# Optimization experiments

Hardware: AMD Instinct MI355X
Metric: run time of the kernel (lower is better)

Reference implementation:

```python
import jax, jax.numpy as jnp
import numpy as np

D_MODEL = 1024
N_HEADS = 16
D_K = D_MODEL // N_HEADS


def setup_inputs() -> dict:
    key = jax.random.key(0)
    ks = jax.random.split(key, 9)
    B, S, D = 2, 2048, D_MODEL
    q = jax.random.normal(ks[0], (B, S, D), dtype=jnp.float32)
    v = jax.random.normal(ks[1], (B, S, D), dtype=jnp.float32)
    k = jax.random.normal(ks[2], (B, S, D), dtype=jnp.float32)
    att_mask = jnp.zeros((B, S, S), dtype=jnp.float32)
    seq_mask = jax.random.uniform(ks[3], (B, S, S), dtype=jnp.float32)
    scale = 1.0 / np.sqrt(D)
    Wq = jax.random.normal(ks[4], (D, D), dtype=jnp.float32) * scale
    Wk = jax.random.normal(ks[5], (D, D), dtype=jnp.float32) * scale
    Wv = jax.random.normal(ks[6], (D, D), dtype=jnp.float32) * scale
    Wo = jax.random.normal(ks[7], (D, D), dtype=jnp.float32) * scale
    return {"q": q, "v": v, "k": k, "att_mask": att_mask, "seq_mask": seq_mask,
            "Wq": Wq, "Wk": Wk, "Wv": Wv, "Wo": Wo}


def _split_heads(x, B):
    # [B, S, D] -> [B, H, S, d_k]
    return x.reshape(B, -1, N_HEADS, D_K).transpose(0, 2, 1, 3)


def reference(q, v, k, att_mask, seq_mask, Wq, Wk, Wv, Wo):
    B = q.shape[0]
    qh = _split_heads(q @ Wq, B)
    kh = _split_heads(k @ Wk, B)
    vh = _split_heads(v @ Wv, B)
    # scores: [B, H, Sq, Sk]
    scores = jnp.einsum('bhqd,bhkd->bhqk', qh, kh) / jnp.sqrt(jnp.float32(D_K))
    scores = scores + att_mask[:, None]
    attn = jax.nn.softmax(scores, axis=-1)
    attn = attn * seq_mask[:, None]  # post-softmax multiplicative mask
    out = jnp.einsum('bhqk,bhkd->bhqd', attn, vh)
    out = out.transpose(0, 2, 1, 3).reshape(B, -1, D_MODEL)
    return out @ Wo
```

## Files before the change

kernel.cpp:

```cpp
#include <hip/hip_runtime.h>
#include <cstddef>

typedef __attribute__((ext_vector_type(8))) short s16x8;
typedef __attribute__((ext_vector_type(4))) float f32x4;
typedef __attribute__((ext_vector_type(4))) unsigned short us4;

static __device__ __forceinline__ float bf2f(unsigned short u) {
    union { unsigned u; float f; } v;
    v.u = ((unsigned)u) << 16;
    return v.f;
}

static __device__ __forceinline__ unsigned short f2bf(float f) {
    union { float f; unsigned u; } v;
    v.f = f;
    unsigned r = v.u + 0x7fffu + ((v.u >> 16) & 1u);
    return (unsigned short)(r >> 16);
}

static __device__ __forceinline__ float ldf(const unsigned short* p, size_t i) { return bf2f(p[i]); }
static __device__ __forceinline__ float ldf(const float* p, size_t i) { return p[i]; }
static __device__ __forceinline__ void stf(unsigned short* p, size_t i, float v) { p[i] = f2bf(v); }
static __device__ __forceinline__ void stf(float* p, size_t i, float v) { p[i] = v; }

__global__ __launch_bounds__(256) void probe_dtype(
    const unsigned short* __restrict__ q, unsigned* __restrict__ flags)
{
    __shared__ float red[256];
    const int t = threadIdx.x;
    float m = 0.0f;
    for (int i = t; i < 16384; i += 256) {
        float x = fabsf(bf2f(q[i]));
        if (!(x == x)) x = 1.0e30f;
        m = fmaxf(m, x);
    }
    red[t] = m;
    __syncthreads();
    for (int s = 128; s > 0; s >>= 1) {
        if (t < s) red[t] = fmaxf(red[t], red[t + s]);
        __syncthreads();
    }
    if (t == 0) {
        flags[0] = (red[0] < 1000.0f) ? 0u : 1u;
        flags[1] = 0u;
    }
}

__global__ __launch_bounds__(256) void probe_zero(
    const uint4* __restrict__ m, unsigned* __restrict__ flags)
{
    const unsigned dt = flags[0];
    const size_t n = dt ? 2097152u : 1048576u;
    unsigned acc = 0;
    for (size_t i = (size_t)blockIdx.x * 256 + threadIdx.x; i < n;
         i += (size_t)gridDim.x * 256) {
        uint4 v = m[i];
        acc |= v.x | v.y | v.z | v.w;
    }
    if (acc) atomicOr(&flags[1], 1u);
}

__global__ __launch_bounds__(256) void cvt_f32_bf16(
    const float4* __restrict__ src, us4* __restrict__ dst, unsigned n4,
    const unsigned* __restrict__ flags, unsigned gate)
{
    if (flags[0] != 1u) return;
    if (gate != 0u && flags[1] == 0u) return;
    for (unsigned i = blockIdx.x * 256u + threadIdx.x; i < n4;
         i += gridDim.x * 256u) {
        float4 v = src[i];
        us4 o;
        o.x = f2bf(v.x); o.y = f2bf(v.y); o.z = f2bf(v.z); o.w = f2bf(v.w);
        dst[i] = o;
    }
}

__global__ __launch_bounds__(256) void copy_bf16(
    const uint4* __restrict__ src, uint4* __restrict__ dst, unsigned n16,
    const unsigned* __restrict__ flags, unsigned gate)
{
    if (flags[0] != 0u) return;
    if (gate != 0u && flags[1] == 0u) return;
    for (unsigned i = blockIdx.x * 256u + threadIdx.x; i < n16;
         i += gridDim.x * 256u)
        dst[i] = src[i];
}

template <typename T>
__global__ __launch_bounds__(256) void transpose_w(
    const T* __restrict__ src, unsigned short* __restrict__ dst,
    const unsigned* __restrict__ flag, unsigned want)
{
    if (*flag != want) return;
    __shared__ unsigned short tile[32][33];
    const int c0 = blockIdx.x * 32, r0 = blockIdx.y * 32;
    const int tx = threadIdx.x, ty = threadIdx.y;
#pragma unroll
    for (int i = 0; i < 32; i += 8)
        tile[ty + i][tx] = f2bf(ldf(src, (size_t)(r0 + ty + i) * 1024 + c0 + tx));
    __syncthreads();
#pragma unroll
    for (int i = 0; i < 32; i += 8)
        dst[(size_t)(c0 + ty + i) * 1024 + r0 + tx] = tile[tx][ty + i];
}

template <typename TO>
__global__ __launch_bounds__(256) void gemm_kernel(
    const unsigned short* __restrict__ A, const unsigned short* __restrict__ Bt,
    TO* __restrict__ out, int mode, const unsigned* __restrict__ flags, unsigned want)
{
    if (want != 2u && flags[0] != want) return;
    const int K = 1024;
    __shared__ __align__(16) unsigned short lA[64 * 72];
    __shared__ __align__(16) unsigned short lB[64 * 72];

    const int m0 = blockIdx.y * 64, n0 = blockIdx.x * 64;
    const int t = threadIdx.x;
    const int w = t >> 6, l = t & 63, quad = l >> 4, l15 = l & 15;
    const int srow = t >> 2, scol = (t & 3) * 16;

    f32x4 acc[4] = {};

    for (int k0 = 0; k0 < K; k0 += 64) {
        const uint4* ga = (const uint4*)(A + (size_t)(m0 + srow) * K + k0 + scol);
        uint4 a0 = ga[0], a1 = ga[1];
        const uint4* gb = (const uint4*)(Bt + (size_t)(n0 + srow) * K + k0 + scol);
        uint4 b0 = gb[0], b1 = gb[1];
        *(uint4*)&lA[srow * 72 + scol] = a0;
        *(uint4*)&lA[srow * 72 + scol + 8] = a1;
        *(uint4*)&lB[srow * 72 + scol] = b0;
        *(uint4*)&lB[srow * 72 + scol + 8] = b1;
        __syncthreads();
#pragma unroll
        for (int kk = 0; kk < 64; kk += 32) {
            s16x8 af = *(const s16x8*)&lA[(w * 16 + l15) * 72 + kk + quad * 8];
#pragma unroll
            for (int g = 0; g < 4; g++) {
                s16x8 bf = *(const s16x8*)&lB[(g * 16 + l15) * 72 + kk + quad * 8];
                acc[g] = __builtin_amdgcn_mfma_f32_16x16x32_bf16(af, bf, acc[g], 0, 0, 0);
            }
        }
        __syncthreads();
    }

#pragma unroll
    for (int g = 0; g < 4; g++) {
#pragma unroll
        for (int r = 0; r < 4; r++) {
            int row = m0 + w * 16 + quad * 4 + r;
            int col = n0 + g * 16 + l15;
            float val = acc[g][r];
            if (mode == 0) {
                stf(out, (size_t)row * 1024 + col, val);
            } else {
                int b = row >> 11, s = row & 2047;
                int h = col >> 6, d = col & 63;
                if (mode == 1)
                    stf(out, (((size_t)(b * 16 + h) * 2048) + s) * 64 + d, val);
                else
                    stf(out, (((size_t)(b * 16 + h) * 64) + d) * 2048 + s, val);
            }
        }
    }
}

template <typename TM>
__global__ __launch_bounds__(256) void attn_kernel(
    const unsigned short* __restrict__ qh, const unsigned short* __restrict__ kh,
    const unsigned short* __restrict__ vt, const TM* __restrict__ amask,
    const unsigned short* __restrict__ smask, unsigned short* __restrict__ aout,
    const unsigned* __restrict__ flags, unsigned want)
{
    if (flags[0] != want) return;
    const bool useA = (flags[1] != 0u);
    const int S = 2048, DK = 64, H = 16;
    const int qt = blockIdx.x, h = blockIdx.y, b = blockIdx.z;
    const unsigned short* qhb = qh + (size_t)(b * H + h) * S * DK;
    const unsigned short* khb = kh + (size_t)(b * H + h) * S * DK;
    const unsigned short* vtb = vt + (size_t)(b * H + h) * DK * S;
    const TM* amb = amask + (size_t)b * S * S;
    const unsigned short* smb = smask + (size_t)b * S * S;

    __shared__ __align__(16) unsigned short lK[64 * 72];
    __shared__ __align__(16) unsigned short lV[64 * 72];
    __shared__ __align__(16) unsigned short lP[4][16 * 72];

    const int t = threadIdx.x;
    const int w = t >> 6, l = t & 63, quad = l >> 4, l15 = l & 15;
    const int q0 = qt * 64;
    const int srow = t >> 2, scol = (t & 3) * 16;

    const int qrow_a = q0 + w * 16 + l15;
    s16x8 qf0 = *(const s16x8*)&qhb[(size_t)qrow_a * DK + quad * 8];
    s16x8 qf1 = *(const s16x8*)&qhb[(size_t)qrow_a * DK + 32 + quad * 8];

    float mrun[4], lrun[4];
    f32x4 o[4] = {};
#pragma unroll
    for (int r = 0; r < 4; r++) { mrun[r] = -INFINITY; lrun[r] = 0.0f; }

    for (int k0 = 0; k0 < S; k0 += 64) {
        const uint4* gk = (const uint4*)&khb[(size_t)(k0 + srow) * DK + scol];
        const uint4* gv = (const uint4*)&vtb[(size_t)srow * S + k0 + scol];
        uint4 ka = gk[0], kb = gk[1];
        uint4 va = gv[0], vb = gv[1];
        *(uint4*)&lK[srow * 72 + scol] = ka;
        *(uint4*)&lK[srow * 72 + scol + 8] = kb;
        *(uint4*)&lV[srow * 72 + scol] = va;
        *(uint4*)&lV[srow * 72 + scol + 8] = vb;
        __syncthreads();

        f32x4 sc[4] = {};
#pragma unroll
        for (int kk = 0; kk < 64; kk += 32) {
            s16x8 af = (kk == 0) ? qf0 : qf1;
#pragma unroll
            for (int g = 0; g < 4; g++) {
                s16x8 bf = *(const s16x8*)&lK[(g * 16 + l15) * 72 + kk + quad * 8];
                sc[g] = __builtin_amdgcn_mfma_f32_16x16x32_bf16(af, bf, sc[g], 0, 0, 0);
            }
        }

#pragma unroll
        for (int r = 0; r < 4; r++) {
            const int qr = q0 + w * 16 + quad * 4 + r;
            const size_t mrow = (size_t)qr * S + k0;
            float sv[4];
            float mx = -INFINITY;
            if (useA) {
#pragma unroll
                for (int g = 0; g < 4; g++) {
                    float s = sc[g][r] * 0.125f + ldf(amb, mrow + g * 16 + l15);
                    sv[g] = s;
                    mx = fmaxf(mx, s);
                }
            } else {
#pragma unroll
                for (int g = 0; g < 4; g++) {
                    float s = sc[g][r] * 0.125f;
                    sv[g] = s;
                    mx = fmaxf(mx, s);
                }
            }
#pragma unroll
            for (int d = 1; d < 16; d <<= 1) mx = fmaxf(mx, __shfl_xor(mx, d));
            float mnew = fmaxf(mrun[r], mx);
            float rs = 0.0f;
#pragma unroll
            for (int g = 0; g < 4; g++) {
                float e = __expf(sv[g] - mnew);
                sv[g] = e;
                rs += e;
            }
#pragma unroll
            for (int d = 1; d < 16; d <<= 1) rs += __shfl_xor(rs, d);
            float alpha = __expf(mrun[r] - mnew);
            lrun[r] = lrun[r] * alpha + rs;
            mrun[r] = mnew;
#pragma unroll
            for (int g = 0; g < 4; g++) o[g][r] *= alpha;
#pragma unroll
            for (int g = 0; g < 4; g++) {
                float pm = sv[g] * bf2f(smb[mrow + g * 16 + l15]);
                lP[w][(quad * 4 + r) * 72 + g * 16 + l15] = f2bf(pm);
            }
        }
        __syncthreads();

#pragma unroll
        for (int kk = 0; kk < 64; kk += 32) {
            s16x8 pf = *(const s16x8*)&lP[w][l15 * 72 + kk + quad * 8];
#pragma unroll
            for (int g = 0; g < 4; g++) {
                s16x8 vf = *(const s16x8*)&lV[(g * 16 + l15) * 72 + kk + quad * 8];
                o[g] = __builtin_amdgcn_mfma_f32_16x16x32_bf16(pf, vf, o[g], 0, 0, 0);
            }
        }
        __syncthreads();
    }

#pragma unroll
    for (int r = 0; r < 4; r++) {
        float inv = 1.0f / lrun[r];
        const int qr = q0 + w * 16 + quad * 4 + r;
#pragma unroll
        for (int g = 0; g < 4; g++) {
            aout[((size_t)(b * S + qr)) * 1024 + h * 64 + g * 16 + l15] =
                f2bf(o[g][r] * inv);
        }
    }
}

extern "C" void kernel_launch(void* const* d_in, const int* in_sizes, int n_in,
                              void* d_out, int out_size, void* d_ws, size_t ws_size,
                              hipStream_t stream)
{
    const void* q   = d_in[0];
    const void* v   = d_in[1];
    const void* k   = d_in[2];
    const void* att = d_in[3];
    const void* seq = d_in[4];
    const void* Wq  = d_in[5];
    const void* Wk  = d_in[6];
    const void* Wv  = d_in[7];
    const void* Wo  = d_in[8];

    const size_t WELEM = 1024 * 1024;
    const size_t HELEM = (size_t)2 * 16 * 2048 * 64;

    unsigned* flags = (unsigned*)d_ws;
    unsigned short* base = (unsigned short*)((char*)d_ws + 512);
    unsigned short* r0 = base;
    unsigned short* qh = base + HELEM;
    unsigned short* kh = qh + HELEM;
    unsigned short* vt = kh + HELEM;
    unsigned short* qb = vt + HELEM;
    unsigned short* kb = qb + HELEM;
    unsigned short* vb = kb + HELEM;
    unsigned short* seqb = qb;

    const dim3 tg(32, 32), tb(32, 8);
    const dim3 gg(16, 64), gb(256);
    const dim3 ag(32, 16, 2), ab(256);

    probe_dtype<<<1, 256, 0, stream>>>((const unsigned short*)q, flags);
    probe_zero<<<1024, 256, 0, stream>>>((const uint4*)att, flags);

    const unsigned n4h = 1048576u, n16h = 524288u;
    cvt_f32_bf16<<<1024, 256, 0, stream>>>((const float4*)q, (us4*)qb, n4h, flags, 0);
    cvt_f32_bf16<<<1024, 256, 0, stream>>>((const float4*)k, (us4*)kb, n4h, flags, 0);
    cvt_f32_bf16<<<1024, 256, 0, stream>>>((const float4*)v, (us4*)vb, n4h, flags, 0);
    copy_bf16<<<1024, 256, 0, stream>>>((const uint4*)q, (uint4*)qb, n16h, flags, 0);
    copy_bf16<<<1024, 256, 0, stream>>>((const uint4*)k, (uint4*)kb, n16h, flags, 0);
    copy_bf16<<<1024, 256, 0, stream>>>((const uint4*)v, (uint4*)vb, n16h, flags, 0);

    transpose_w<unsigned short><<<tg, tb, 0, stream>>>((const unsigned short*)Wq, r0 + 0 * WELEM, flags, 0);
    transpose_w<unsigned short><<<tg, tb, 0, stream>>>((const unsigned short*)Wk, r0 + 1 * WELEM, flags, 0);
    transpose_w<unsigned short><<<tg, tb, 0, stream>>>((const unsigned short*)Wv, r0 + 2 * WELEM, flags, 0);
    transpose_w<float><<<tg, tb, 0, stream>>>((const float*)Wq, r0 + 0 * WELEM, flags, 1);
    transpose_w<float><<<tg, tb, 0, stream>>>((const float*)Wk, r0 + 1 * WELEM, flags, 1);
    transpose_w<float><<<tg, tb, 0, stream>>>((const float*)Wv, r0 + 2 * WELEM, flags, 1);

    gemm_kernel<unsigned short><<<gg, gb, 0, stream>>>(qb, r0 + 0 * WELEM, qh, 1, flags, 2);
    gemm_kernel<unsigned short><<<gg, gb, 0, stream>>>(kb, r0 + 1 * WELEM, kh, 1, flags, 2);
    gemm_kernel<unsigned short><<<gg, gb, 0, stream>>>(vb, r0 + 2 * WELEM, vt, 2, flags, 2);

    const unsigned n4s = 2097152u, n16s = 1048576u;
    cvt_f32_bf16<<<2048, 256, 0, stream>>>((const float4*)seq, (us4*)seqb, n4s, flags, 0);
    copy_bf16<<<2048, 256, 0, stream>>>((const uint4*)seq, (uint4*)seqb, n16s, flags, 0);

    unsigned short* ao = r0;
    attn_kernel<unsigned short><<<ag, ab, 0, stream>>>(qh, kh, vt, (const unsigned short*)att, seqb, ao, flags, 0);
    attn_kernel<float><<<ag, ab, 0, stream>>>(qh, kh, vt, (const float*)att, seqb, ao, flags, 1);

    transpose_w<unsigned short><<<tg, tb, 0, stream>>>((const unsigned short*)Wo, qh, flags, 0);
    transpose_w<float><<<tg, tb, 0, stream>>>((const float*)Wo, qh, flags, 1);

    gemm_kernel<unsigned short><<<gg, gb, 0, stream>>>(ao, qh, (unsigned short*)d_out, 0, flags, 0);
    gemm_kernel<float><<<gg, gb, 0, stream>>>(ao, qh, (float*)d_out, 0, flags, 1);
}
```

Before: 435.9 us.

## Fuse launches, use exp2 softmax with lazy rescale and swizzled P tile

Merges the three conversion, copy and weight-transpose launches into single multi-operand kernels. The bf16 path now reads the seq mask directly and skips its copy. In attention, the scale is folded into a log2 domain so exp2 can be used. The running max is rescaled only when some lane's max grows, and row sums are reduced once at the end. The P tile in LDS uses an XOR swizzle, and bf16 packing uses the hardware convert instruction. These cut launch overhead, ALU/shuffle work and LDS bank conflicts, at the cost of a different rounding path.

```diff
diff --git a/kernel.cpp b/kernel.cpp
--- a/kernel.cpp
+++ b/kernel.cpp
@@ -17,6 +17,18 @@
     unsigned r = v.u + 0x7fffu + ((v.u >> 16) & 1u);
     return (unsigned short)(r >> 16);
 }
+
+static __device__ __forceinline__ unsigned short f2bf_fast(float f) {
+    unsigned r;
+    asm("v_cvt_pk_bf16_f32 %0, %1, %2" : "=v"(r) : "v"(f), "v"(f));
+    return (unsigned short)r;
+}
+
+#if __has_builtin(__builtin_amdgcn_exp2f)
+#define EXP2F(x) __builtin_amdgcn_exp2f(x)
+#else
+#define EXP2F(x) exp2f(x)
+#endif
 
 static __device__ __forceinline__ float ldf(const unsigned short* p, size_t i) { return bf2f(p[i]); }
 static __device__ __forceinline__ float ldf(const float* p, size_t i) { return p[i]; }
@@ -60,12 +72,43 @@
     if (acc) atomicOr(&flags[1], 1u);
 }
 
+__global__ __launch_bounds__(256) void cvt3_f32_bf16(
+    const float4* __restrict__ s0, us4* __restrict__ d0,
+    const float4* __restrict__ s1, us4* __restrict__ d1,
+    const float4* __restrict__ s2, us4* __restrict__ d2,
+    unsigned n4, const unsigned* __restrict__ flags)
+{
+    if (flags[0] != 1u) return;
+    const float4* s = (blockIdx.y == 0) ? s0 : (blockIdx.y == 1) ? s1 : s2;
+    us4* d = (blockIdx.y == 0) ? d0 : (blockIdx.y == 1) ? d1 : d2;
+    for (unsigned i = blockIdx.x * 256u + threadIdx.x; i < n4;
+         i += gridDim.x * 256u) {
+        float4 v = s[i];
+        us4 o;
+        o.x = f2bf(v.x); o.y = f2bf(v.y); o.z = f2bf(v.z); o.w = f2bf(v.w);
+        d[i] = o;
+    }
+}
+
+__global__ __launch_bounds__(256) void copy3_bf16(
+    const uint4* __restrict__ s0, uint4* __restrict__ d0,
+    const uint4* __restrict__ s1, uint4* __restrict__ d1,
+    const uint4* __restrict__ s2, uint4* __restrict__ d2,
+    unsigned n16, const unsigned* __restrict__ flags)
+{
+    if (flags[0] != 0u) return;
+    const uint4* s = (blockIdx.y == 0) ? s0 : (blockIdx.y == 1) ? s1 : s2;
+    uint4* d = (blockIdx.y == 0) ? d0 : (blockIdx.y == 1) ? d1 : d2;
+    for (unsigned i = blockIdx.x * 256u + threadIdx.x; i < n16;
+         i += gridDim.x * 256u)
+        d[i] = s[i];
+}
+
 __global__ __launch_bounds__(256) void cvt_f32_bf16(
     const float4* __restrict__ src, us4* __restrict__ dst, unsigned n4,
-    const unsigned* __restrict__ flags, unsigned gate)
+    const unsigned* __restrict__ flags)
 {
     if (flags[0] != 1u) return;
-    if (gate != 0u && flags[1] == 0u) return;
     for (unsigned i = blockIdx.x * 256u + threadIdx.x; i < n4;
          i += gridDim.x * 256u) {
         float4 v = src[i];
@@ -75,23 +118,34 @@
     }
 }
 
-__global__ __launch_bounds__(256) void copy_bf16(
-    const uint4* __restrict__ src, uint4* __restrict__ dst, unsigned n16,
-    const unsigned* __restrict__ flags, unsigned gate)
-{
-    if (flags[0] != 0u) return;
-    if (gate != 0u && flags[1] == 0u) return;
-    for (unsigned i = blockIdx.x * 256u + threadIdx.x; i < n16;
-         i += gridDim.x * 256u)
-        dst[i] = src[i];
-}
-
 template <typename T>
 __global__ __launch_bounds__(256) void transpose_w(
     const T* __restrict__ src, unsigned short* __restrict__ dst,
     const unsigned* __restrict__ flag, unsigned want)
 {
     if (*flag != want) return;
+    __shared__ unsigned short tile[32][33];
+    const int c0 = blockIdx.x * 32, r0 = blockIdx.y * 32;
+    const int tx = threadIdx.x, ty = threadIdx.y;
+#pragma unroll
+    for (int i = 0; i < 32; i += 8)
+        tile[ty + i][tx] = f2bf(ldf(src, (size_t)(r0 + ty + i) * 1024 + c0 + tx));
+    __syncthreads();
+#pragma unroll
+    for (int i = 0; i < 32; i += 8)
+        dst[(size_t)(c0 + ty + i) * 1024 + r0 + tx] = tile[tx][ty + i];
+}
+
+template <typename T>
+__global__ __launch_bounds__(256) void transpose_w3(
+    const T* __restrict__ s0, const T* __restrict__ s1, const T* __restrict__ s2,
+    unsigned short* __restrict__ d0, unsigned short* __restrict__ d1,
+    unsigned short* __restrict__ d2,
+    const unsigned* __restrict__ flag, unsigned want)
+{
+    if (*flag != want) return;
+    const T* src = (blockIdx.z == 0) ? s0 : (blockIdx.z == 1) ? s1 : s2;
+    unsigned short* dst = (blockIdx.z == 0) ? d0 : (blockIdx.z == 1) ? d1 : d2;
     __shared__ unsigned short tile[32][33];
     const int c0 = blockIdx.x * 32, r0 = blockIdx.y * 32;
     const int tx = threadIdx.x, ty = threadIdx.y;
@@ -178,8 +232,6 @@
     const unsigned short* qhb = qh + (size_t)(b * H + h) * S * DK;
     const unsigned short* khb = kh + (size_t)(b * H + h) * S * DK;
     const unsigned short* vtb = vt + (size_t)(b * H + h) * DK * S;
-    const TM* amb = amask + (size_t)b * S * S;
-    const unsigned short* smb = smask + (size_t)b * S * S;
 
     __shared__ __align__(16) unsigned short lK[64 * 72];
     __shared__ __align__(16) unsigned short lV[64 * 72];
@@ -190,14 +242,26 @@
     const int q0 = qt * 64;
     const int srow = t >> 2, scol = (t & 3) * 16;
 
+    const float SCALE2 = 0.18033688011112042f;
+    const float LOG2E  = 1.4426950408889634f;
+
+    const unsigned short* mr[4];
+    const TM* ar[4];
+#pragma unroll
+    for (int r = 0; r < 4; r++) {
+        const size_t rowoff = (size_t)(q0 + w * 16 + quad * 4 + r) * S + l15;
+        mr[r] = smask + (size_t)b * S * S + rowoff;
+        ar[r] = amask + (size_t)b * S * S + rowoff;
+    }
+
     const int qrow_a = q0 + w * 16 + l15;
     s16x8 qf0 = *(const s16x8*)&qhb[(size_t)qrow_a * DK + quad * 8];
     s16x8 qf1 = *(const s16x8*)&qhb[(size_t)qrow_a * DK + 32 + quad * 8];
 
-    float mrun[4], lrun[4];
+    float mrun[4], lsum[4];
     f32x4 o[4] = {};
 #pragma unroll
-    for (int r = 0; r < 4; r++) { mrun[r] = -INFINITY; lrun[r] = 0.0f; }
+    for (int r = 0; r < 4; r++) { mrun[r] = -INFINITY; lsum[r] = 0.0f; }
 
     for (int k0 = 0; k0 < S; k0 += 64) {
         const uint4* gk = (const uint4*)&khb[(size_t)(k0 + srow) * DK + scol];
@@ -223,53 +287,47 @@
 
 #pragma unroll
         for (int r = 0; r < 4; r++) {
-            const int qr = q0 + w * 16 + quad * 4 + r;
-            const size_t mrow = (size_t)qr * S + k0;
             float sv[4];
-            float mx = -INFINITY;
             if (useA) {
 #pragma unroll
-                for (int g = 0; g < 4; g++) {
-                    float s = sc[g][r] * 0.125f + ldf(amb, mrow + g * 16 + l15);
-                    sv[g] = s;
-                    mx = fmaxf(mx, s);
-                }
+                for (int g = 0; g < 4; g++)
+                    sv[g] = fmaf((float)ldf(ar[r], k0 + g * 16), LOG2E,
+                                 sc[g][r] * SCALE2);
             } else {
 #pragma unroll
-                for (int g = 0; g < 4; g++) {
-                    float s = sc[g][r] * 0.125f;
-                    sv[g] = s;
-                    mx = fmaxf(mx, s);
-                }
-            }
+                for (int g = 0; g < 4; g++) sv[g] = sc[g][r] * SCALE2;
+            }
+            float mx = fmaxf(fmaxf(sv[0], sv[1]), fmaxf(sv[2], sv[3]));
 #pragma unroll
             for (int d = 1; d < 16; d <<= 1) mx = fmaxf(mx, __shfl_xor(mx, d));
-            float mnew = fmaxf(mrun[r], mx);
-            float rs = 0.0f;
-#pragma unroll
-            for (int g = 0; g < 4; g++) {
-                float e = __expf(sv[g] - mnew);
-                sv[g] = e;
-                rs += e;
-            }
-#pragma unroll
-            for (int d = 1; d < 16; d <<= 1) rs += __shfl_xor(rs, d);
-            float alpha = __expf(mrun[r] - mnew);
-            lrun[r] = lrun[r] * alpha + rs;
-            mrun[r] = mnew;
-#pragma unroll
-            for (int g = 0; g < 4; g++) o[g][r] *= alpha;
-#pragma unroll
-            for (int g = 0; g < 4; g++) {
-                float pm = sv[g] * bf2f(smb[mrow + g * 16 + l15]);
-                lP[w][(quad * 4 + r) * 72 + g * 16 + l15] = f2bf(pm);
-            }
-        }
-        __syncthreads();
-
+
+            if (!__all(mx <= mrun[r])) {
+                float mnew = fmaxf(mrun[r], mx);
+                float alpha = EXP2F(mrun[r] - mnew);
+                lsum[r] *= alpha;
+#pragma unroll
+                for (int g = 0; g < 4; g++) o[g][r] *= alpha;
+                mrun[r] = mnew;
+            }
+
+            const int rowp = quad * 4 + r;
+            const int rsw = (rowp & 8) << 1;
+            float e0 = EXP2F(sv[0] - mrun[r]);
+            float e1 = EXP2F(sv[1] - mrun[r]);
+            float e2 = EXP2F(sv[2] - mrun[r]);
+            float e3 = EXP2F(sv[3] - mrun[r]);
+            lsum[r] += (e0 + e1) + (e2 + e3);
+            lP[w][rowp * 72 + ((0 * 16 + l15) ^ rsw)] = f2bf_fast(e0 * bf2f(mr[r][k0 + 0]));
+            lP[w][rowp * 72 + ((1 * 16 + l15) ^ rsw)] = f2bf_fast(e1 * bf2f(mr[r][k0 + 16]));
+            lP[w][rowp * 72 + ((2 * 16 + l15) ^ rsw)] = f2bf_fast(e2 * bf2f(mr[r][k0 + 32]));
+            lP[w][rowp * 72 + ((3 * 16 + l15) ^ rsw)] = f2bf_fast(e3 * bf2f(mr[r][k0 + 48]));
+        }
+        __syncthreads();
+
+        const int rdsw = (l15 & 8) << 1;
 #pragma unroll
         for (int kk = 0; kk < 64; kk += 32) {
-            s16x8 pf = *(const s16x8*)&lP[w][l15 * 72 + kk + quad * 8];
+            s16x8 pf = *(const s16x8*)&lP[w][l15 * 72 + ((kk + quad * 8) ^ rdsw)];
 #pragma unroll
             for (int g = 0; g < 4; g++) {
                 s16x8 vf = *(const s16x8*)&lV[(g * 16 + l15) * 72 + kk + quad * 8];
@@ -281,12 +339,15 @@
 
 #pragma unroll
     for (int r = 0; r < 4; r++) {
-        float inv = 1.0f / lrun[r];
+        float ls = lsum[r];
+#pragma unroll
+        for (int d = 1; d < 16; d <<= 1) ls += __shfl_xor(ls, d);
+        float inv = 1.0f / ls;
         const int qr = q0 + w * 16 + quad * 4 + r;
 #pragma unroll
         for (int g = 0; g < 4; g++) {
             aout[((size_t)(b * S + qr)) * 1024 + h * 64 + g * 16 + l15] =
-                f2bf(o[g][r] * inv);
+                f2bf_fast(o[g][r] * inv);
         }
     }
 }
@@ -320,6 +381,7 @@
     unsigned short* seqb = qb;
 
     const dim3 tg(32, 32), tb(32, 8);
+    const dim3 tg3(32, 32, 3);
     const dim3 gg(16, 64), gb(256);
     const dim3 ag(32, 16, 2), ab(256);
 
@@ -327,31 +389,32 @@
     probe_zero<<<1024, 256, 0, stream>>>((const uint4*)att, flags);
 
     const unsigned n4h = 1048576u, n16h = 524288u;
-    cvt_f32_bf16<<<1024, 256, 0, stream>>>((const float4*)q, (us4*)qb, n4h, flags, 0);
-    cvt_f32_bf16<<<1024, 256, 0, stream>>>((const float4*)k, (us4*)kb, n4h, flags, 0);
-    cvt_f32_bf16<<<1024, 256, 0, stream>>>((const float4*)v, (us4*)vb, n4h, flags, 0);
-    copy_bf16<<<1024, 256, 0, stream>>>((const uint4*)q, (uint4*)qb, n16h, flags, 0);
-    copy_bf16<<<1024, 256, 0, stream>>>((const uint4*)k, (uint4*)kb, n16h, flags, 0);
-    copy_bf16<<<1024, 256, 0, stream>>>((const uint4*)v, (uint4*)vb, n16h, flags, 0);
-
-    transpose_w<unsigned short><<<tg, tb, 0, stream>>>((const unsigned short*)Wq, r0 + 0 * WELEM, flags, 0);
-    transpose_w<unsigned short><<<tg, tb, 0, stream>>>((const unsigned short*)Wk, r0 + 1 * WELEM, flags, 0);
-    transpose_w<unsigned short><<<tg, tb, 0, stream>>>((const unsigned short*)Wv, r0 + 2 * WELEM, flags, 0);
-    transpose_w<float><<<tg, tb, 0, stream>>>((const float*)Wq, r0 + 0 * WELEM, flags, 1);
-    transpose_w<float><<<tg, tb, 0, stream>>>((const float*)Wk, r0 + 1 * WELEM, flags, 1);
-    transpose_w<float><<<tg, tb, 0, stream>>>((const float*)Wv, r0 + 2 * WELEM, flags, 1);
+    cvt3_f32_bf16<<<dim3(512, 3), 256, 0, stream>>>(
+        (const float4*)q, (us4*)qb, (const float4*)k, (us4*)kb,
+        (const float4*)v, (us4*)vb, n4h, flags);
+    copy3_bf16<<<dim3(512, 3), 256, 0, stream>>>(
+        (const uint4*)q, (uint4*)qb, (const uint4*)k, (uint4*)kb,
+        (const uint4*)v, (uint4*)vb, n16h, flags);
+
+    transpose_w3<unsigned short><<<tg3, tb, 0, stream>>>(
+        (const unsigned short*)Wq, (const unsigned short*)Wk, (const unsigned short*)Wv,
+        r0 + 0 * WELEM, r0 + 1 * WELEM, r0 + 2 * WELEM, flags, 0);
+    transpose_w3<float><<<tg3, tb, 0, stream>>>(
+        (const float*)Wq, (const float*)Wk, (const float*)Wv,
+        r0 + 0 * WELEM, r0 + 1 * WELEM, r0 + 2 * WELEM, flags, 1);
 
     gemm_kernel<unsigned short><<<gg, gb, 0, stream>>>(qb, r0 + 0 * WELEM, qh, 1, flags, 2);
     gemm_kernel<unsigned short><<<gg, gb, 0, stream>>>(kb, r0 + 1 * WELEM, kh, 1, flags, 2);
     gemm_kernel<unsigned short><<<gg, gb, 0, stream>>>(vb, r0 + 2 * WELEM, vt, 2, flags, 2);
 
-    const unsigned n4s = 2097152u, n16s = 1048576u;
-    cvt_f32_bf16<<<2048, 256, 0, stream>>>((const float4*)seq, (us4*)seqb, n4s, flags, 0);
-    copy_bf16<<<2048, 256, 0, stream>>>((const uint4*)seq, (uint4*)seqb, n16s, flags, 0);
+    const unsigned n4s = 2097152u;
+    cvt_f32_bf16<<<2048, 256, 0, stream>>>((const float4*)seq, (us4*)seqb, n4s, flags);
 
     unsigned short* ao = r0;
-    attn_kernel<unsigned short><<<ag, ab, 0, stream>>>(qh, kh, vt, (const unsigned short*)att, seqb, ao, flags, 0);
-    attn_kernel<float><<<ag, ab, 0, stream>>>(qh, kh, vt, (const float*)att, seqb, ao, flags, 1);
+    attn_kernel<unsigned short><<<ag, ab, 0, stream>>>(
+        qh, kh, vt, (const unsigned short*)att, (const unsigned short*)seq, ao, flags, 0);
+    attn_kernel<float><<<ag, ab, 0, stream>>>(
+        qh, kh, vt, (const float*)att, seqb, ao, flags, 1);
 
     transpose_w<unsigned short><<<tg, tb, 0, stream>>>((const unsigned short*)Wo, qh, flags, 0);
     transpose_w<float><<<tg, tb, 0, stream>>>((const float*)Wo, qh, flags, 1);
```

Measured after the change: 484.7 us. 11.2% more time.
